# Performance work log

Hardware: AMD Instinct MI355X
Metric: run time of the kernel (lower is better)

## Reference

```python
import jax, jax.numpy as jnp
import numpy as np

B, F, V, E = 16384, 20, 100000, 32
D_BOT = F * E            # 640
DIMS = (512, 256)        # bottom MLP dims
TDIMS = (128, 64)        # tower hidden dims
N_DOM = 4


def setup_inputs() -> dict:
    key = jax.random.key(0)
    ks = jax.random.split(key, 16)
    inp = {
        "feature_ids": jax.random.randint(ks[0], (B, F), 0, V, dtype=jnp.int64),
        "domain_id": jax.random.randint(ks[1], (B,), 0, N_DOM, dtype=jnp.int64),
        # embedding tables [F, V, E]
        "emb": jax.random.normal(ks[2], (F, V, E), dtype=jnp.float32) * 0.01,
        # bottom MLP: 640 -> 512 -> 256 (relu, no output layer)
        "W1": jax.random.normal(ks[3], (D_BOT, DIMS[0]), dtype=jnp.float32) * (1.0 / np.sqrt(D_BOT)),
        "b1": jnp.zeros((DIMS[0],), dtype=jnp.float32),
        "W2": jax.random.normal(ks[4], (DIMS[0], DIMS[1]), dtype=jnp.float32) * (1.0 / np.sqrt(DIMS[0])),
        "b2": jnp.zeros((DIMS[1],), dtype=jnp.float32),
        # towers (stacked over domain dim): 256 -> 128 -> 64 -> 1
        "TW1": jax.random.normal(ks[5], (N_DOM, DIMS[1], TDIMS[0]), dtype=jnp.float32) * (1.0 / np.sqrt(DIMS[1])),
        "Tb1": jnp.zeros((N_DOM, TDIMS[0]), dtype=jnp.float32),
        "TW2": jax.random.normal(ks[6], (N_DOM, TDIMS[0], TDIMS[1]), dtype=jnp.float32) * (1.0 / np.sqrt(TDIMS[0])),
        "Tb2": jnp.zeros((N_DOM, TDIMS[1]), dtype=jnp.float32),
        "TW3": jax.random.normal(ks[7], (N_DOM, TDIMS[1], 1), dtype=jnp.float32) * (1.0 / np.sqrt(TDIMS[1])),
        "Tb3": jnp.zeros((N_DOM, 1), dtype=jnp.float32),
    }
    return inp


def reference(feature_ids, domain_id, emb, W1, b1, W2, b2, TW1, Tb1, TW2, Tb2, TW3, Tb3):
    # Embedding lookup + concat: [B, F, E] -> [B, F*E]
    e = emb[jnp.arange(F)[None, :], feature_ids]          # [B, F, E]
    h = e.reshape(B, F * E)
    # Shared bottom MLP (relu)
    h = jax.nn.relu(h @ W1 + b1)                          # [B, 512]
    h = jax.nn.relu(h @ W2 + b2)                          # [B, 256]
    # All domain towers computed densely for every sample (faithful to source)
    t = jax.nn.relu(jnp.einsum('bi,dio->bdo', h, TW1) + Tb1[None])   # [B, D, 128]
    t = jax.nn.relu(jnp.einsum('bdi,dio->bdo', t, TW2) + Tb2[None])  # [B, D, 64]
    logit = jnp.einsum('bdi,dio->bdo', t, TW3) + Tb3[None]           # [B, D, 1]
    ys = jax.nn.sigmoid(logit)[..., 0]                    # [B, D]
    # Select per-sample domain output via mask (domains are exclusive)
    onehot = jax.nn.one_hot(domain_id, N_DOM, dtype=ys.dtype)        # [B, D]
    final = jnp.sum(ys * onehot, axis=1)                  # [B]
    return final
```

## Files before the change

kernel.cpp:

```cpp
#include <hip/hip_runtime.h>

#define B_SZ  16384
#define F_SZ  20
#define V_SZ  100000
#define E_SZ  32
#define DBOT  640
#define D1    512
#define D2    256
#define T1D   128
#define T2D   64
#define NDOM  4

typedef __bf16 bf16x8 __attribute__((ext_vector_type(8)));
typedef float  f32x4  __attribute__((ext_vector_type(4)));

#define MFMA(a, b, c) __builtin_amdgcn_mfma_f32_16x16x32_bf16((a), (b), (c), 0, 0, 0)

__global__ __launch_bounds__(256) void k_prep(const float* __restrict__ W1,
                                              const float* __restrict__ W2,
                                              const float* __restrict__ TW1,
                                              const float* __restrict__ TW2,
                                              __bf16* __restrict__ W1P,
                                              __bf16* __restrict__ W2P,
                                              __bf16* __restrict__ TW1P,
                                              __bf16* __restrict__ TW2P) {
  int bid = blockIdx.x, tid = threadIdx.x;
  const float* src; __bf16* dst; int n, k, N;
  if (bid < 160) {
    long g = (long)bid * 256 + tid;
    int lane = g & 63; int kkg = (int)((g >> 6) % 20); int ntile = (int)(g / 1280);
    n = ntile * 16 + (lane & 15); k = kkg * 32 + ((lane >> 4) << 3);
    src = W1; N = D1; dst = W1P + g * 8;
  } else if (bid < 224) {
    long g = (long)(bid - 160) * 256 + tid;
    int lane = g & 63; int kkg = (int)((g >> 6) & 15); int ntile = (int)(g >> 10);
    n = ntile * 16 + (lane & 15); k = kkg * 32 + ((lane >> 4) << 3);
    src = W2; N = D2; dst = W2P + g * 8;
  } else if (bid < 288) {
    long g = (long)(bid - 224) * 256 + tid;
    int d = (int)(g >> 12); long r = g & 4095;
    int lane = r & 63; int kkg = (int)((r >> 6) & 7); int ntile = (int)(r >> 9);
    n = ntile * 16 + (lane & 15); k = kkg * 32 + ((lane >> 4) << 3);
    src = TW1 + (long)d * D2 * T1D; N = T1D;
    dst = TW1P + ((long)(d * 64 + ntile * 8 + kkg) * 64 + lane) * 8;
  } else {
    long g = (long)(bid - 288) * 256 + tid;
    int d = (int)(g >> 10); long r = g & 1023;
    int lane = r & 63; int kkg = (int)((r >> 6) & 3); int ntile = (int)(r >> 8);
    n = ntile * 16 + (lane & 15); k = kkg * 32 + ((lane >> 4) << 3);
    src = TW2 + (long)d * T1D * T2D; N = T2D;
    dst = TW2P + ((long)(d * 16 + ntile * 4 + kkg) * 64 + lane) * 8;
  }
  bf16x8 o;
#pragma unroll
  for (int e = 0; e < 8; ++e) o[e] = (__bf16)src[(long)(k + e) * N + n];
  *(bf16x8*)dst = o;
}

__global__ __launch_bounds__(512) void k_mega(const int* __restrict__ fids,
                                              const int* __restrict__ dom,
                                              const float* __restrict__ emb,
                                              const __bf16* __restrict__ W1P,
                                              const float* __restrict__ b1,
                                              const __bf16* __restrict__ W2P,
                                              const float* __restrict__ b2,
                                              const __bf16* __restrict__ TW1P,
                                              const __bf16* __restrict__ TW2P,
                                              const float* __restrict__ Tb1,
                                              const float* __restrict__ Tb2,
                                              const float* __restrict__ TW3,
                                              const float* __restrict__ Tb3,
                                              float* __restrict__ out) {
  __shared__ __attribute__((aligned(16))) char smem[152576];
  int*    ids_lds = (int*)(smem + 147456);
  __bf16* sA      = (__bf16*)smem;
  __bf16* h1      = (__bf16*)(smem + 81920);
  __bf16* h2_lds  = (__bf16*)smem;
  __bf16* t_lds   = (__bf16*)(smem + 81920);

  int bid = blockIdx.x, tid = threadIdx.x;
  int lane = tid & 63, w = tid >> 6;
  int lrow = lane & 15, kq = lane >> 4;
  int m0 = bid * 64;

  for (int i = tid; i < 64 * F_SZ; i += 512) ids_lds[i] = fids[m0 * F_SZ + i];
  __syncthreads();

  {
    float4 ga[10], gb[10];
    int sb[10];
#pragma unroll
    for (int i = 0; i < 10; ++i) {
      unsigned c = tid + i * 512;
      unsigned row = c / 80;
      unsigned cc = c - row * 80;
      int f = cc >> 2, es = (cc & 3) << 3;
      int id = ids_lds[row * F_SZ + f];
      const float* p = emb + ((long)f * V_SZ + id) * E_SZ + es;
      ga[i] = *(const float4*)p;
      gb[i] = *(const float4*)(p + 4);
      sb[i] = (int)(row * 1280 + cc * 16) ^ ((row & 7) << 4);
    }
#pragma unroll
    for (int i = 0; i < 10; ++i) {
      bf16x8 o;
      o[0] = (__bf16)ga[i].x; o[1] = (__bf16)ga[i].y;
      o[2] = (__bf16)ga[i].z; o[3] = (__bf16)ga[i].w;
      o[4] = (__bf16)gb[i].x; o[5] = (__bf16)gb[i].y;
      o[6] = (__bf16)gb[i].z; o[7] = (__bf16)gb[i].w;
      *(bf16x8*)((char*)sA + sb[i]) = o;
    }
  }
  __syncthreads();

  {
    f32x4 acc[4][4] = {};
#pragma unroll
    for (int f = 0; f < F_SZ; ++f) {
      bf16x8 af[4];
#pragma unroll
      for (int mi = 0; mi < 4; ++mi) {
        int byte = ((mi * 16 + lrow) * 1280 + (f * 32 + kq * 8) * 2) ^ ((lrow & 7) << 4);
        af[mi] = *(const bf16x8*)((const char*)sA + byte);
      }
#pragma unroll
      for (int ni = 0; ni < 4; ++ni) {
        bf16x8 bfr = *(const bf16x8*)(W1P +
            ((long)((w * 4 + ni) * 20 + f) * 64 + lane) * 8);
#pragma unroll
        for (int mi = 0; mi < 4; ++mi)
          acc[mi][ni] = MFMA(af[mi], bfr, acc[mi][ni]);
      }
    }
#pragma unroll
    for (int ni = 0; ni < 4; ++ni) {
      int col = w * 64 + ni * 16 + lrow;
      float bv = b1[col];
#pragma unroll
      for (int mi = 0; mi < 4; ++mi) {
#pragma unroll
        for (int r = 0; r < 4; ++r) {
          int row = mi * 16 + kq * 4 + r;
          float v = acc[mi][ni][r] + bv;
          v = v > 0.f ? v : 0.f;
          int byte = (row * 1024 + col * 2) ^ ((row & 7) << 4);
          *(__bf16*)((char*)h1 + byte) = (__bf16)v;
        }
      }
    }
  }
  __syncthreads();

  {
    f32x4 acc2[4][2] = {};
#pragma unroll 4
    for (int kkg = 0; kkg < 16; ++kkg) {
      bf16x8 a2[4];
#pragma unroll
      for (int mi = 0; mi < 4; ++mi) {
        int byte = ((mi * 16 + lrow) * 1024 + kkg * 64 + kq * 16) ^ ((lrow & 7) << 4);
        a2[mi] = *(const bf16x8*)((const char*)h1 + byte);
      }
#pragma unroll
      for (int ni = 0; ni < 2; ++ni) {
        bf16x8 bfr = *(const bf16x8*)(W2P +
            ((long)((w * 2 + ni) * 16 + kkg) * 64 + lane) * 8);
#pragma unroll
        for (int mi = 0; mi < 4; ++mi)
          acc2[mi][ni] = MFMA(a2[mi], bfr, acc2[mi][ni]);
      }
    }
#pragma unroll
    for (int ni = 0; ni < 2; ++ni) {
      int col = w * 32 + ni * 16 + lrow;
      float bv = b2[col];
#pragma unroll
      for (int mi = 0; mi < 4; ++mi) {
#pragma unroll
        for (int r = 0; r < 4; ++r) {
          int row = mi * 16 + kq * 4 + r;
          float v = acc2[mi][ni][r] + bv;
          v = v > 0.f ? v : 0.f;
          int byte = (row * 512 + col * 2) ^ ((row & 7) << 4);
          *(__bf16*)((char*)h2_lds + byte) = (__bf16)v;
        }
      }
    }
  }
  __syncthreads();

  {
    int d  = w >> 1;
    int r0 = (w & 1) * 32;
    __bf16* tw = t_lds + w * 4096;

    bf16x8 a1[2][8];
#pragma unroll
    for (int mi = 0; mi < 2; ++mi)
#pragma unroll
      for (int kk = 0; kk < 8; ++kk) {
        int row = r0 + mi * 16 + lrow;
        int byte = (row * 512 + (kk * 32 + kq * 8) * 2) ^ ((row & 7) << 4);
        a1[mi][kk] = *(const bf16x8*)((const char*)h2_lds + byte);
      }

    f32x4 acc1[2][8] = {};
#pragma unroll
    for (int kk = 0; kk < 8; ++kk) {
#pragma unroll
      for (int ni = 0; ni < 8; ++ni) {
        bf16x8 b = *(const bf16x8*)(TW1P +
            ((long)(d * 64 + ni * 8 + kk) * 64 + lane) * 8);
#pragma unroll
        for (int mi = 0; mi < 2; ++mi)
          acc1[mi][ni] = MFMA(a1[mi][kk], b, acc1[mi][ni]);
      }
    }
#pragma unroll
    for (int ni = 0; ni < 8; ++ni) {
      float bv = Tb1[d * T1D + ni * 16 + lrow];
#pragma unroll
      for (int mi = 0; mi < 2; ++mi) {
#pragma unroll
        for (int r = 0; r < 4; ++r) {
          int lr = mi * 16 + kq * 4 + r;
          float v = acc1[mi][ni][r] + bv;
          v = v > 0.f ? v : 0.f;
          int byte = (lr * 256 + (ni * 16 + lrow) * 2) ^ ((lr & 7) << 4);
          *(__bf16*)((char*)tw + byte) = (__bf16)v;
        }
      }
    }
    asm volatile("s_waitcnt lgkmcnt(0)" ::: "memory");

    bf16x8 a2f[2][4];
#pragma unroll
    for (int mi = 0; mi < 2; ++mi)
#pragma unroll
      for (int kk = 0; kk < 4; ++kk) {
        int lr = mi * 16 + lrow;
        int byte = (lr * 256 + (kk * 32 + kq * 8) * 2) ^ ((lr & 7) << 4);
        a2f[mi][kk] = *(const bf16x8*)((const char*)tw + byte);
      }
    asm volatile("s_waitcnt lgkmcnt(0)" ::: "memory");
    f32x4 acc2[2][4] = {};
#pragma unroll
    for (int kk = 0; kk < 4; ++kk) {
#pragma unroll
      for (int ni = 0; ni < 4; ++ni) {
        bf16x8 b = *(const bf16x8*)(TW2P +
            ((long)(d * 16 + ni * 4 + kk) * 64 + lane) * 8);
#pragma unroll
        for (int mi = 0; mi < 2; ++mi)
          acc2[mi][ni] = MFMA(a2f[mi][kk], b, acc2[mi][ni]);
      }
    }
#pragma unroll
    for (int ni = 0; ni < 4; ++ni) {
      float bv = Tb2[d * T2D + ni * 16 + lrow];
#pragma unroll
      for (int mi = 0; mi < 2; ++mi) {
#pragma unroll
        for (int r = 0; r < 4; ++r) {
          int lr = mi * 16 + kq * 4 + r;
          float v = acc2[mi][ni][r] + bv;
          v = v > 0.f ? v : 0.f;
          int byte = (lr * 128 + (ni * 16 + lrow) * 2) ^ ((lr & 7) << 4);
          *(__bf16*)((char*)tw + byte) = (__bf16)v;
        }
      }
    }
    asm volatile("s_waitcnt lgkmcnt(0)" ::: "memory");

    {
      int lr    = (kq & 1) * 16 + lrow;
      int khalf = kq >> 1;
      float s = 0.f;
#pragma unroll
      for (int j = 0; j < 32; ++j) {
        int col = khalf * 32 + j;
        int byte = (lr * 128 + col * 2) ^ ((lr & 7) << 4);
        s += (float)*(const __bf16*)((const char*)tw + byte) * TW3[d * T2D + col];
      }
      s += __shfl_xor(s, 32);
      s += Tb3[d];
      int grow = r0 + lr;
      if (khalf == 0 && dom[m0 + grow] == d)
        out[m0 + grow] = 1.0f / (1.0f + expf(-s));
    }
  }
}

extern "C" void kernel_launch(void* const* d_in, const int* in_sizes, int n_in,
                              void* d_out, int out_size, void* d_ws, size_t ws_size,
                              hipStream_t stream) {
  const int*   fids = (const int*)d_in[0];
  const int*   dom  = (const int*)d_in[1];
  const float* emb  = (const float*)d_in[2];
  const float* W1   = (const float*)d_in[3];
  const float* b1   = (const float*)d_in[4];
  const float* W2   = (const float*)d_in[5];
  const float* b2   = (const float*)d_in[6];
  const float* TW1  = (const float*)d_in[7];
  const float* Tb1  = (const float*)d_in[8];
  const float* TW2  = (const float*)d_in[9];
  const float* Tb2  = (const float*)d_in[10];
  const float* TW3  = (const float*)d_in[11];
  const float* Tb3  = (const float*)d_in[12];
  float* out = (float*)d_out;

  char* ws = (char*)d_ws;
  __bf16* W1P   = (__bf16*)(ws);
  __bf16* W2P   = (__bf16*)(ws + 655360);
  __bf16* TW1P  = (__bf16*)(ws + 917504);
  __bf16* TW2P  = (__bf16*)(ws + 1179648);

  k_prep<<<304, 256, 0, stream>>>(W1, W2, TW1, TW2, W1P, W2P, TW1P, TW2P);
  k_mega<<<256, 512, 0, stream>>>(fids, dom, emb, W1P, b1, W2P, b2,
                                  TW1P, TW2P, Tb1, Tb2, TW3, Tb3, out);
}
```

Measured before the change: 47.10 us.

## Pipeline embedding gather with first GEMM in feature groups of four

The embedding gather is split into five stages of four features each. Each stage's global loads are issued before the MFMAs for the previous stage, so gather latency overlaps the first-layer matmul, with manual barriers and sched_barriers enforcing the order. W1 fragments for a group are preloaded into registers. This lowers live registers compared with holding all 10 gathers at once, but adds four extra block barriers. Correctness depends on the LDS write/read ordering, since each stage writes distinct columns of sA.

```diff
diff --git a/kernel.cpp b/kernel.cpp
--- a/kernel.cpp
+++ b/kernel.cpp
@@ -86,37 +86,66 @@
   for (int i = tid; i < 64 * F_SZ; i += 512) ids_lds[i] = fids[m0 * F_SZ + i];
   __syncthreads();
 
+  int row0 = tid >> 4,          cc0 = tid & 15;
+  int row1 = (tid + 512) >> 4,  cc1 = tid & 15;
+  int sb0 = (row0 * 1280 + cc0 * 16) ^ ((row0 & 7) << 4);
+  int sb1 = (row1 * 1280 + cc1 * 16) ^ ((row1 & 7) << 4);
+  int f0base = cc0 >> 2, es0 = (cc0 & 3) << 3;
+  int f1base = cc1 >> 2, es1 = (cc1 & 3) << 3;
+
+  float4 g0a, g0b, g1a, g1b;
   {
-    float4 ga[10], gb[10];
-    int sb[10];
-#pragma unroll
-    for (int i = 0; i < 10; ++i) {
-      unsigned c = tid + i * 512;
-      unsigned row = c / 80;
-      unsigned cc = c - row * 80;
-      int f = cc >> 2, es = (cc & 3) << 3;
-      int id = ids_lds[row * F_SZ + f];
-      const float* p = emb + ((long)f * V_SZ + id) * E_SZ + es;
-      ga[i] = *(const float4*)p;
-      gb[i] = *(const float4*)(p + 4);
-      sb[i] = (int)(row * 1280 + cc * 16) ^ ((row & 7) << 4);
-    }
-#pragma unroll
-    for (int i = 0; i < 10; ++i) {
+    int f = f0base;
+    int id = ids_lds[row0 * F_SZ + f];
+    const float* p = emb + ((long)f * V_SZ + id) * E_SZ + es0;
+    g0a = *(const float4*)p; g0b = *(const float4*)(p + 4);
+    f = f1base;
+    id = ids_lds[row1 * F_SZ + f];
+    const float* q = emb + ((long)f * V_SZ + id) * E_SZ + es1;
+    g1a = *(const float4*)q; g1b = *(const float4*)(q + 4);
+  }
+
+  f32x4 acc[4][4] = {};
+
+#pragma unroll
+  for (int g = 0; g < 5; ++g) {
+    {
       bf16x8 o;
-      o[0] = (__bf16)ga[i].x; o[1] = (__bf16)ga[i].y;
-      o[2] = (__bf16)ga[i].z; o[3] = (__bf16)ga[i].w;
-      o[4] = (__bf16)gb[i].x; o[5] = (__bf16)gb[i].y;
-      o[6] = (__bf16)gb[i].z; o[7] = (__bf16)gb[i].w;
-      *(bf16x8*)((char*)sA + sb[i]) = o;
-    }
-  }
-  __syncthreads();
-
-  {
-    f32x4 acc[4][4] = {};
-#pragma unroll
-    for (int f = 0; f < F_SZ; ++f) {
+      o[0] = (__bf16)g0a.x; o[1] = (__bf16)g0a.y; o[2] = (__bf16)g0a.z; o[3] = (__bf16)g0a.w;
+      o[4] = (__bf16)g0b.x; o[5] = (__bf16)g0b.y; o[6] = (__bf16)g0b.z; o[7] = (__bf16)g0b.w;
+      *(bf16x8*)((char*)sA + sb0 + g * 256) = o;
+      o[0] = (__bf16)g1a.x; o[1] = (__bf16)g1a.y; o[2] = (__bf16)g1a.z; o[3] = (__bf16)g1a.w;
+      o[4] = (__bf16)g1b.x; o[5] = (__bf16)g1b.y; o[6] = (__bf16)g1b.z; o[7] = (__bf16)g1b.w;
+      *(bf16x8*)((char*)sA + sb1 + g * 256) = o;
+    }
+    asm volatile("s_waitcnt lgkmcnt(0)" ::: "memory");
+    __builtin_amdgcn_s_barrier();
+    __builtin_amdgcn_sched_barrier(0);
+
+    bf16x8 bfr[4][4];
+#pragma unroll
+    for (int f4 = 0; f4 < 4; ++f4)
+#pragma unroll
+      for (int ni = 0; ni < 4; ++ni)
+        bfr[f4][ni] = *(const bf16x8*)(W1P +
+            ((long)((w * 4 + ni) * 20 + g * 4 + f4) * 64 + lane) * 8);
+    __builtin_amdgcn_sched_barrier(0);
+
+    if (g < 4) {
+      int f = (g + 1) * 4 + f0base;
+      int id = ids_lds[row0 * F_SZ + f];
+      const float* p = emb + ((long)f * V_SZ + id) * E_SZ + es0;
+      g0a = *(const float4*)p; g0b = *(const float4*)(p + 4);
+      f = (g + 1) * 4 + f1base;
+      id = ids_lds[row1 * F_SZ + f];
+      const float* q = emb + ((long)f * V_SZ + id) * E_SZ + es1;
+      g1a = *(const float4*)q; g1b = *(const float4*)(q + 4);
+    }
+    __builtin_amdgcn_sched_barrier(0);
+
+#pragma unroll
+    for (int f4 = 0; f4 < 4; ++f4) {
+      int f = g * 4 + f4;
       bf16x8 af[4];
 #pragma unroll
       for (int mi = 0; mi < 4; ++mi) {
@@ -124,28 +153,26 @@
         af[mi] = *(const bf16x8*)((const char*)sA + byte);
       }
 #pragma unroll
-      for (int ni = 0; ni < 4; ++ni) {
-        bf16x8 bfr = *(const bf16x8*)(W1P +
-            ((long)((w * 4 + ni) * 20 + f) * 64 + lane) * 8);
+      for (int ni = 0; ni < 4; ++ni)
 #pragma unroll
         for (int mi = 0; mi < 4; ++mi)
-          acc[mi][ni] = MFMA(af[mi], bfr, acc[mi][ni]);
-      }
-    }
-#pragma unroll
-    for (int ni = 0; ni < 4; ++ni) {
-      int col = w * 64 + ni * 16 + lrow;
-      float bv = b1[col];
-#pragma unroll
-      for (int mi = 0; mi < 4; ++mi) {
-#pragma unroll
-        for (int r = 0; r < 4; ++r) {
-          int row = mi * 16 + kq * 4 + r;
-          float v = acc[mi][ni][r] + bv;
-          v = v > 0.f ? v : 0.f;
-          int byte = (row * 1024 + col * 2) ^ ((row & 7) << 4);
-          *(__bf16*)((char*)h1 + byte) = (__bf16)v;
-        }
+          acc[mi][ni] = MFMA(af[mi], bfr[f4][ni], acc[mi][ni]);
+    }
+  }
+
+#pragma unroll
+  for (int ni = 0; ni < 4; ++ni) {
+    int col = w * 64 + ni * 16 + lrow;
+    float bv = b1[col];
+#pragma unroll
+    for (int mi = 0; mi < 4; ++mi) {
+#pragma unroll
+      for (int r = 0; r < 4; ++r) {
+        int row = mi * 16 + kq * 4 + r;
+        float v = acc[mi][ni][r] + bv;
+        v = v > 0.f ? v : 0.f;
+        int byte = (row * 1024 + col * 2) ^ ((row & 7) << 4);
+        *(__bf16*)((char*)h1 + byte) = (__bf16)v;
       }
     }
   }
@@ -163,11 +190,11 @@
       }
 #pragma unroll
       for (int ni = 0; ni < 2; ++ni) {
-        bf16x8 bfr = *(const bf16x8*)(W2P +
+        bf16x8 bfr2 = *(const bf16x8*)(W2P +
             ((long)((w * 2 + ni) * 16 + kkg) * 64 + lane) * 8);
 #pragma unroll
         for (int mi = 0; mi < 4; ++mi)
-          acc2[mi][ni] = MFMA(a2[mi], bfr, acc2[mi][ni]);
+          acc2[mi][ni] = MFMA(a2[mi], bfr2, acc2[mi][ni]);
       }
     }
 #pragma unroll
```

New measurement: 44.10 us (median of 3 runs). -6.4%, faster.
